# Kernel tuning notes

Measured on AMD Instinct MI355X. Metric: run time of the kernel, lower is better.

Reference implementation:

```python
import jax, jax.numpy as jnp
import numpy as np

B, H, S, D = 2, 16, 2048, 64
DILATION_RATE = 2

def dilated_global_mask(seq_len: int, dilation_rate: int) -> jnp.ndarray:
    # mask[i, j] = 1 if |i - j| % dilation_rate == 0 else 0  -> [S, S] float32
    i = jnp.arange(seq_len)[:, None]
    j = jnp.arange(seq_len)[None, :]
    return ((jnp.abs(i - j) % dilation_rate) == 0).astype(jnp.float32)

def setup_inputs() -> dict:
    key = jax.random.key(0)
    kq, kk, kv = jax.random.split(key, 3)
    queries = jax.random.normal(kq, (B, H, S, D), dtype=jnp.float32)
    keys = jax.random.normal(kk, (B, H, S, D), dtype=jnp.float32)
    values = jax.random.normal(kv, (B, H, S, D), dtype=jnp.float32)
    return {"queries": queries, "keys": keys, "values": values}

def reference(queries, keys, values):
    depth = queries.shape[-1]
    # scores: [B, H, S, S]
    scores = jnp.einsum("bhqd,bhkd->bhqk", queries, keys)
    scores = scores / jnp.sqrt(jnp.asarray(depth, dtype=jnp.float32))
    gmask = dilated_global_mask(keys.shape[-2], DILATION_RATE)  # [S, S]
    # NOTE: multiplicative masking (masked scores become 0, not -inf), as in source
    masked_scores = scores * gmask
    attention_probs = jax.nn.softmax(masked_scores, axis=-1)
    # dropout is identity at inference (training=None)
    out = jnp.einsum("bhqk,bhkd->bhqd", attention_probs, values)
    return out
```

## Files before the change

### kernel.cpp

```cpp
#include <hip/hip_runtime.h>
#include <hip/hip_bf16.h>


#define B_   2
#define H_   16
#define S_   2048
#define D_   64
#define SP_  1024
#define BQ   64
#define BK   64
#define NKT  (SP_ / BK)

#define QSCALE 0.180336884f

#if __has_builtin(__builtin_amdgcn_exp2f)
#define EXP2(x) __builtin_amdgcn_exp2f(x)
#else
#define EXP2(x) exp2f(x)
#endif

typedef __bf16 bf16x8 __attribute__((ext_vector_type(8)));
typedef __bf16 bf16x4 __attribute__((ext_vector_type(4)));
typedef float  f32x4  __attribute__((ext_vector_type(4)));
typedef short  s16x4  __attribute__((ext_vector_type(4)));

static __device__ __forceinline__ f32x4 mfma16(bf16x4 a, bf16x4 b, f32x4 c) {
    return __builtin_amdgcn_mfma_f32_16x16x16bf16_1k(
        __builtin_bit_cast(s16x4, a), __builtin_bit_cast(s16x4, b), c, 0, 0, 0);
}

#define KSW(r, c8) ((((c8) ^ ((r) & 7)) << 3))

__global__ __launch_bounds__(256) void conv_kernel(const float* __restrict__ K,
                                                   const float* __restrict__ V,
                                                   __bf16* __restrict__ Kbf,
                                                   __bf16* __restrict__ Vt,
                                                   float* __restrict__ vsp) {
    const int bp  = blockIdx.x;
    const int kc  = blockIdx.y;
    const int bh  = bp >> 1;
    const int par = bp & 1;
    const int tid = threadIdx.x;
    const float* Kb = K + (size_t)bh * S_ * D_;
    const float* Vb = V + (size_t)bh * S_ * D_;

    __shared__ __align__(16) __bf16 vt[64][80];
    const int row = tid >> 2;
    const int c0  = (tid & 3) * 16;
    const int c8  = (tid & 3) * 2;

    float vsum = 0.f;
    #pragma unroll
    for (int st2 = 0; st2 < 2; ++st2) {
        const int ktile = kc * 2 + st2;
        const int k0 = ktile * 64;
        {
            const float* ks = Kb + (size_t)(par + 2 * (k0 + row)) * D_ + c0;
            const float4 a0 = *(const float4*)(ks);
            const float4 a1 = *(const float4*)(ks + 4);
            const float4 a2 = *(const float4*)(ks + 8);
            const float4 a3 = *(const float4*)(ks + 12);
            bf16x8 w0, w1;
            w0[0] = (__bf16)a0.x; w0[1] = (__bf16)a0.y;
            w0[2] = (__bf16)a0.z; w0[3] = (__bf16)a0.w;
            w0[4] = (__bf16)a1.x; w0[5] = (__bf16)a1.y;
            w0[6] = (__bf16)a1.z; w0[7] = (__bf16)a1.w;
            w1[0] = (__bf16)a2.x; w1[1] = (__bf16)a2.y;
            w1[2] = (__bf16)a2.z; w1[3] = (__bf16)a2.w;
            w1[4] = (__bf16)a3.x; w1[5] = (__bf16)a3.y;
            w1[6] = (__bf16)a3.z; w1[7] = (__bf16)a3.w;
            __bf16* kdst = Kbf + ((size_t)bp * SP_ + k0 + row) * D_;
            *(bf16x8*)&kdst[KSW(row, c8)]     = w0;
            *(bf16x8*)&kdst[KSW(row, c8 + 1)] = w1;
        }
        {
            const float* vsrc = Vb + (size_t)(par + 2 * (k0 + row)) * D_ + c0;
            const float4 a0 = *(const float4*)(vsrc);
            const float4 a1 = *(const float4*)(vsrc + 4);
            const float4 a2 = *(const float4*)(vsrc + 8);
            const float4 a3 = *(const float4*)(vsrc + 12);
            bf16x8 w0, w1;
            w0[0] = (__bf16)a0.x; w0[1] = (__bf16)a0.y;
            w0[2] = (__bf16)a0.z; w0[3] = (__bf16)a0.w;
            w0[4] = (__bf16)a1.x; w0[5] = (__bf16)a1.y;
            w0[6] = (__bf16)a1.z; w0[7] = (__bf16)a1.w;
            w1[0] = (__bf16)a2.x; w1[1] = (__bf16)a2.y;
            w1[2] = (__bf16)a2.z; w1[3] = (__bf16)a2.w;
            w1[4] = (__bf16)a3.x; w1[5] = (__bf16)a3.y;
            w1[6] = (__bf16)a3.z; w1[7] = (__bf16)a3.w;
            *(bf16x8*)&vt[row][c0]     = w0;
            *(bf16x8*)&vt[row][c0 + 8] = w1;
        }
        __syncthreads();
        {
            const int d = row;
            #pragma unroll
            for (int cc2 = 0; cc2 < 2; ++cc2) {
                const int cc = c8 + cc2;
                bf16x8 w;
                float s = 0.f;
                #pragma unroll
                for (int j = 0; j < 8; ++j) {
                    w[j] = vt[cc * 8 + j][d];
                    s += (float)w[j];
                }
                vsum += s;
                __bf16* vdst = Vt + (((size_t)bp * 16 + ktile) * D_ + d) * 64;
                *(bf16x8*)&vdst[KSW(d, cc)] = w;
            }
        }
        __syncthreads();
    }
    vsum += __shfl_down(vsum, 1);
    vsum += __shfl_down(vsum, 2);
    if ((tid & 3) == 0) vsp[((size_t)bp * 8 + blockIdx.y) * 64 + row] = vsum;
}

__global__ __launch_bounds__(256, 4) void attn3_kernel(const float* __restrict__ Q,
                                                       const __bf16* __restrict__ Kbf,
                                                       const __bf16* __restrict__ Vt,
                                                       const float* __restrict__ vsp,
                                                       float* __restrict__ out) {
    const int bh  = blockIdx.x;
    const int par = blockIdx.y;
    const int qt  = blockIdx.z;
    const int bp  = bh * 2 + par;
    const int tid  = threadIdx.x;
    const int lane = tid & 63;
    const int wave = tid >> 6;
    const int l15  = lane & 15;
    const int quad = lane >> 4;

    __shared__ __align__(16) char arena[32768];
    __bf16 (*kbuf)[BK][64] = (__bf16 (*)[BK][64])arena;
    __bf16 (*vbuf)[D_][64] = (__bf16 (*)[D_][64])(arena + 16384);

    const size_t base = (size_t)bh * S_ * D_;

    bf16x8 qf[2];
    {
        const int qrow = qt * BQ + wave * 16 + l15;
        const float* qsrc = Q + base + (size_t)(par + 2 * qrow) * D_ + quad * 8;
        #pragma unroll
        for (int ks = 0; ks < 2; ++ks) {
            const float4 a = *(const float4*)(qsrc + ks * 32);
            const float4 b = *(const float4*)(qsrc + ks * 32 + 4);
            bf16x8 w;
            w[0] = (__bf16)(a.x * QSCALE); w[1] = (__bf16)(a.y * QSCALE);
            w[2] = (__bf16)(a.z * QSCALE); w[3] = (__bf16)(a.w * QSCALE);
            w[4] = (__bf16)(b.x * QSCALE); w[5] = (__bf16)(b.y * QSCALE);
            w[6] = (__bf16)(b.z * QSCALE); w[7] = (__bf16)(b.w * QSCALE);
            qf[ks] = w;
        }
    }

    const uint4* Kt4 = (const uint4*)(Kbf + (size_t)bp * SP_ * D_);
    const uint4* Vt4 = (const uint4*)(Vt  + (size_t)bp * SP_ * D_);
    uint4 sk0, sk1, sv0, sv1;

    auto issue_loads = [&](int kt) {
        const int o = kt * 512 + tid;
        sk0 = Kt4[o]; sk1 = Kt4[o + 256];
        sv0 = Vt4[o]; sv1 = Vt4[o + 256];
    };
    auto stage = [&](int buf) {
        uint4* kd = (uint4*)kbuf[buf];
        uint4* vd = (uint4*)vbuf[buf];
        kd[tid] = sk0; kd[tid + 256] = sk1;
        vd[tid] = sv0; vd[tid + 256] = sv1;
    };

    issue_loads(0);
    stage(0);
    __syncthreads();

    f32x4 acc[4];
    #pragma unroll
    for (int dt = 0; dt < 4; ++dt) acc[dt] = (f32x4){0.f, 0.f, 0.f, 0.f};
    float l_acc = 0.f;

    for (int kt = 0; kt < NKT; ++kt) {
        const int cur = kt & 1;
        const bool pf = (kt + 1 < NKT);

        if (pf) issue_loads(kt + 1);

        const __bf16 (*kb)[64] = kbuf[cur];
        const __bf16 (*vb)[64] = vbuf[cur];

        bf16x8 ka[2][4];
        #pragma unroll
        for (int ks = 0; ks < 2; ++ks)
            #pragma unroll
            for (int kt4 = 0; kt4 < 4; ++kt4) {
                const int R = kt4 * 16 + l15;
                ka[ks][kt4] = *(const bf16x8*)&kb[R][KSW(R, ks * 4 + quad)];
            }
        bf16x4 va[4][4];
        #pragma unroll
        for (int dt = 0; dt < 4; ++dt) {
            const int R = dt * 16 + l15;
            const int ro = R & 7;
            #pragma unroll
            for (int kt4 = 0; kt4 < 4; ++kt4) {
                const int ch = (kt4 * 2 + (quad >> 1)) ^ ro;
                va[kt4][dt] = *(const bf16x4*)&vb[R][ch * 8 + (quad & 1) * 4];
            }
        }

        f32x4 st[4];
        #pragma unroll
        for (int kt4 = 0; kt4 < 4; ++kt4) st[kt4] = (f32x4){0.f, 0.f, 0.f, 0.f};
        #pragma unroll
        for (int ks = 0; ks < 2; ++ks)
            #pragma unroll
            for (int kt4 = 0; kt4 < 4; ++kt4)
                st[kt4] = __builtin_amdgcn_mfma_f32_16x16x32_bf16(
                    ka[ks][kt4], qf[ks], st[kt4], 0, 0, 0);
        #pragma unroll
        for (int kt4 = 0; kt4 < 4; ++kt4) {
            const float p0 = EXP2(st[kt4][0]);
            const float p1 = EXP2(st[kt4][1]);
            const float p2 = EXP2(st[kt4][2]);
            const float p3 = EXP2(st[kt4][3]);
            l_acc += (p0 + p1) + (p2 + p3);
            bf16x4 pb;
            pb[0] = (__bf16)p0; pb[1] = (__bf16)p1;
            pb[2] = (__bf16)p2; pb[3] = (__bf16)p3;
            #pragma unroll
            for (int dt = 0; dt < 4; ++dt)
                acc[dt] = mfma16(va[kt4][dt], pb, acc[dt]);
        }

        if (pf) stage(1 - cur);
        __syncthreads();
    }

    float Z = l_acc;
    Z += __shfl_xor(Z, 16);
    Z += __shfl_xor(Z, 32);
    const float rz = 1.0f / (Z + 1024.0f);

    const float* vsb = vsp + (size_t)(bh * 2 + (1 - par)) * 8 * 64;
    f32x4 vs4[4];
    #pragma unroll
    for (int dt = 0; dt < 4; ++dt) {
        f32x4 s = (f32x4){0.f, 0.f, 0.f, 0.f};
        #pragma unroll
        for (int kc = 0; kc < 8; ++kc)
            s += *(const f32x4*)&vsb[kc * 64 + dt * 16 + quad * 4];
        vs4[dt] = s;
    }

    float* tw = (float*)arena + wave * (16 * 68);
    #pragma unroll
    for (int dt = 0; dt < 4; ++dt) {
        const f32x4 o = (acc[dt] + vs4[dt]) * rz;
        *(f32x4*)&tw[l15 * 68 + dt * 16 + quad * 4] = o;
    }
    #pragma unroll
    for (int i = 0; i < 4; ++i) {
        const int q = i * 4 + quad;
        const f32x4 ov = *(const f32x4*)&tw[q * 68 + l15 * 4];
        const int qg = par + 2 * (qt * BQ + wave * 16 + q);
        *(f32x4*)&out[base + (size_t)qg * D_ + l15 * 4] = ov;
    }
}

__global__ __launch_bounds__(1024) void vsum_kernel(const float* __restrict__ V,
                                                    float* __restrict__ vs) {
    const int bp  = blockIdx.x;
    const int bh  = bp >> 1;
    const int par = bp & 1;
    const int d   = threadIdx.x & 63;
    const int rg  = threadIdx.x >> 6;
    const float* Vb = V + (size_t)bh * S_ * D_;
    float s = 0.f;
    for (int r = rg; r < SP_; r += 16)
        s += Vb[(size_t)(par + 2 * r) * D_ + d];
    __shared__ float red[16][64];
    red[rg][d] = s;
    __syncthreads();
    if (rg == 0) {
        float t = 0.f;
        #pragma unroll
        for (int i = 0; i < 16; ++i) t += red[i][d];
        vs[(size_t)bp * 64 + d] = t;
    }
}

__global__ __launch_bounds__(256, 4) void attn_fb_kernel(const float* __restrict__ Q,
                                                         const float* __restrict__ K,
                                                         const float* __restrict__ V,
                                                         const float* __restrict__ vs,
                                                         float* __restrict__ out) {
    const int bh  = blockIdx.x;
    const int par = blockIdx.y;
    const int qt  = blockIdx.z;
    const int tid  = threadIdx.x;
    const int lane = tid & 63;
    const int wave = tid >> 6;
    const int l15  = lane & 15;
    const int quad = lane >> 4;

    __shared__ __align__(16) char arena[32768];
    __bf16 (*kbuf)[BK][64] = (__bf16 (*)[BK][64])arena;
    __bf16 (*vbuf)[D_][64] = (__bf16 (*)[D_][64])(arena + 16384);

    const size_t base = (size_t)bh * S_ * D_;
    const float* Qb = Q + base;
    const float* Kb = K + base;
    const float* Vb = V + base;

    bf16x8 qf[2];
    {
        const int qrow = qt * BQ + wave * 16 + l15;
        const float* qsrc = Qb + (size_t)(par + 2 * qrow) * D_ + quad * 8;
        #pragma unroll
        for (int ks = 0; ks < 2; ++ks) {
            const float4 a = *(const float4*)(qsrc + ks * 32);
            const float4 b = *(const float4*)(qsrc + ks * 32 + 4);
            bf16x8 w;
            w[0] = (__bf16)(a.x * QSCALE); w[1] = (__bf16)(a.y * QSCALE);
            w[2] = (__bf16)(a.z * QSCALE); w[3] = (__bf16)(a.w * QSCALE);
            w[4] = (__bf16)(b.x * QSCALE); w[5] = (__bf16)(b.y * QSCALE);
            w[6] = (__bf16)(b.z * QSCALE); w[7] = (__bf16)(b.w * QSCALE);
            qf[ks] = w;
        }
    }

    const int kr0 = tid >> 3;
    const int kc8 = tid & 7;
    float4 pka[2], pkb[2];
    float  pv[16];

    auto issue_loads = [&](int kt) {
        #pragma unroll
        for (int i = 0; i < 2; ++i) {
            const int r = i * 32 + kr0;
            const float* ksrc = Kb + (size_t)(par + 2 * (kt * BK + r)) * D_ + kc8 * 8;
            pka[i] = *(const float4*)ksrc;
            pkb[i] = *(const float4*)(ksrc + 4);
        }
        #pragma unroll
        for (int i = 0; i < 2; ++i) {
            const int c = wave + 4 * i;
            const float* vsrc = Vb + (size_t)(par + 2 * (kt * BK + c * 8)) * D_ + lane;
            #pragma unroll
            for (int j = 0; j < 8; ++j)
                pv[i * 8 + j] = vsrc[(size_t)(2 * j) * D_];
        }
    };
    auto stage = [&](int buf) {
        #pragma unroll
        for (int i = 0; i < 2; ++i) {
            const int r = i * 32 + kr0;
            bf16x8 w;
            w[0] = (__bf16)pka[i].x; w[1] = (__bf16)pka[i].y;
            w[2] = (__bf16)pka[i].z; w[3] = (__bf16)pka[i].w;
            w[4] = (__bf16)pkb[i].x; w[5] = (__bf16)pkb[i].y;
            w[6] = (__bf16)pkb[i].z; w[7] = (__bf16)pkb[i].w;
            *(bf16x8*)&kbuf[buf][r][KSW(r, kc8)] = w;
        }
        #pragma unroll
        for (int i = 0; i < 2; ++i) {
            const int c = wave + 4 * i;
            bf16x8 w;
            #pragma unroll
            for (int j = 0; j < 8; ++j) w[j] = (__bf16)pv[i * 8 + j];
            *(bf16x8*)&vbuf[buf][lane][KSW(lane, c)] = w;
        }
    };

    issue_loads(0);
    stage(0);
    __syncthreads();

    f32x4 acc[4];
    #pragma unroll
    for (int dt = 0; dt < 4; ++dt) acc[dt] = (f32x4){0.f, 0.f, 0.f, 0.f};
    float l_acc = 0.f;

    for (int kt = 0; kt < NKT; ++kt) {
        const int cur = kt & 1;
        const bool pf = (kt + 1 < NKT);
        if (pf) issue_loads(kt + 1);

        const __bf16 (*kb)[64] = kbuf[cur];
        const __bf16 (*vb)[64] = vbuf[cur];

        bf16x8 ka[2][4];
        #pragma unroll
        for (int ks = 0; ks < 2; ++ks)
            #pragma unroll
            for (int kt4 = 0; kt4 < 4; ++kt4) {
                const int R = kt4 * 16 + l15;
                ka[ks][kt4] = *(const bf16x8*)&kb[R][KSW(R, ks * 4 + quad)];
            }
        bf16x4 va[4][4];
        #pragma unroll
        for (int dt = 0; dt < 4; ++dt) {
            const int R = dt * 16 + l15;
            const int ro = R & 7;
            #pragma unroll
            for (int kt4 = 0; kt4 < 4; ++kt4) {
                const int ch = (kt4 * 2 + (quad >> 1)) ^ ro;
                va[kt4][dt] = *(const bf16x4*)&vb[R][ch * 8 + (quad & 1) * 4];
            }
        }

        f32x4 st[4];
        #pragma unroll
        for (int kt4 = 0; kt4 < 4; ++kt4) st[kt4] = (f32x4){0.f, 0.f, 0.f, 0.f};
        #pragma unroll
        for (int ks = 0; ks < 2; ++ks)
            #pragma unroll
            for (int kt4 = 0; kt4 < 4; ++kt4)
                st[kt4] = __builtin_amdgcn_mfma_f32_16x16x32_bf16(
                    ka[ks][kt4], qf[ks], st[kt4], 0, 0, 0);
        #pragma unroll
        for (int kt4 = 0; kt4 < 4; ++kt4) {
            const float p0 = EXP2(st[kt4][0]);
            const float p1 = EXP2(st[kt4][1]);
            const float p2 = EXP2(st[kt4][2]);
            const float p3 = EXP2(st[kt4][3]);
            l_acc += (p0 + p1) + (p2 + p3);
            bf16x4 pb;
            pb[0] = (__bf16)p0; pb[1] = (__bf16)p1;
            pb[2] = (__bf16)p2; pb[3] = (__bf16)p3;
            #pragma unroll
            for (int dt = 0; dt < 4; ++dt)
                acc[dt] = mfma16(va[kt4][dt], pb, acc[dt]);
        }

        if (pf) stage(1 - cur);
        __syncthreads();
    }

    float Z = l_acc;
    Z += __shfl_xor(Z, 16);
    Z += __shfl_xor(Z, 32);
    const float rz = 1.0f / (Z + 1024.0f);
    const float* vso = vs + ((size_t)(bh * 2 + (1 - par))) * 64;

    float* tw = (float*)arena + wave * (16 * 68);
    #pragma unroll
    for (int dt = 0; dt < 4; ++dt) {
        const f32x4 vs4 = *(const f32x4*)&vso[dt * 16 + quad * 4];
        const f32x4 o = (acc[dt] + vs4) * rz;
        *(f32x4*)&tw[l15 * 68 + dt * 16 + quad * 4] = o;
    }
    #pragma unroll
    for (int i = 0; i < 4; ++i) {
        const int q = i * 4 + quad;
        const f32x4 ov = *(const f32x4*)&tw[q * 68 + l15 * 4];
        const int qg = par + 2 * (qt * BQ + wave * 16 + q);
        *(f32x4*)&out[base + (size_t)qg * D_ + l15 * 4] = ov;
    }
}

extern "C" void kernel_launch(void* const* d_in, const int* in_sizes, int n_in,
                              void* d_out, int out_size, void* d_ws, size_t ws_size,
                              hipStream_t stream) {
    const float* Q = (const float*)d_in[0];
    const float* K = (const float*)d_in[1];
    const float* V = (const float*)d_in[2];
    float* out = (float*)d_out;

    const size_t KBF_BYTES = (size_t)64 * SP_ * D_ * sizeof(__bf16);
    const size_t VSP_BYTES = (size_t)64 * 8 * 64 * sizeof(float);
    const size_t need = 2 * KBF_BYTES + VSP_BYTES;

    if (ws_size >= need) {
        __bf16* Kbf = (__bf16*)d_ws;
        __bf16* Vt  = (__bf16*)((char*)d_ws + KBF_BYTES);
        float*  vsp = (float*)((char*)d_ws + 2 * KBF_BYTES);
        conv_kernel<<<dim3(64, 8), dim3(256), 0, stream>>>(K, V, Kbf, Vt, vsp);
        attn3_kernel<<<dim3(B_ * H_, 2, SP_ / BQ), dim3(256), 0, stream>>>(
            Q, Kbf, Vt, vsp, out);
    } else {
        float* vsn = (float*)d_ws;
        vsum_kernel<<<dim3(B_ * H_ * 2), dim3(1024), 0, stream>>>(V, vsn);
        attn_fb_kernel<<<dim3(B_ * H_, 2, SP_ / BQ), dim3(256), 0, stream>>>(
            Q, K, V, vsn, out);
    }
}
```

Measured before the change: 125.1 us.

## Use 2-wave blocks with two query sub-tiles per wave and remap grid

The attention kernel now runs 128-thread blocks in which each wave handles 32 query rows as two 16-row sub-tiles. This reuses each K/V fragment read from LDS for twice as many MFMAs, and the staging loop is reorganised so the smaller block still loads the full K/V tile. A 1D grid with a swizzled block-to-(bh,par,qt) mapping spreads neighbouring blocks across head-pairs, and s_setprio raises wave priority around the MFMA section. The cost is higher register pressure from doubled accumulators and fewer waves per block to hide latency.

```diff
diff --git a/kernel.cpp b/kernel.cpp
--- a/kernel.cpp
+++ b/kernel.cpp
@@ -8,6 +8,7 @@
 #define D_   64
 #define SP_  1024
 #define BQ   64
+#define FBQ  64
 #define BK   64
 #define NKT  (SP_ / BK)
 
@@ -116,14 +117,16 @@
     if ((tid & 3) == 0) vsp[((size_t)bp * 8 + blockIdx.y) * 64 + row] = vsum;
 }
 
-__global__ __launch_bounds__(256, 4) void attn3_kernel(const float* __restrict__ Q,
+__global__ __launch_bounds__(128, 2) void attn5_kernel(const float* __restrict__ Q,
                                                        const __bf16* __restrict__ Kbf,
                                                        const __bf16* __restrict__ Vt,
                                                        const float* __restrict__ vsp,
                                                        float* __restrict__ out) {
-    const int bh  = blockIdx.x;
-    const int par = blockIdx.y;
-    const int qt  = blockIdx.z;
+    const int h  = blockIdx.x;
+    const int L  = (h & 7) * 128 + (h >> 3);
+    const int qt  = L & 15;
+    const int par = (L >> 4) & 1;
+    const int bh  = L >> 5;
     const int bp  = bh * 2 + par;
     const int tid  = threadIdx.x;
     const int lane = tid & 63;
@@ -137,9 +140,10 @@
 
     const size_t base = (size_t)bh * S_ * D_;
 
-    bf16x8 qf[2];
-    {
-        const int qrow = qt * BQ + wave * 16 + l15;
+    bf16x8 qf[2][2];
+    #pragma unroll
+    for (int qt2 = 0; qt2 < 2; ++qt2) {
+        const int qrow = qt * BQ + wave * 32 + qt2 * 16 + l15;
         const float* qsrc = Q + base + (size_t)(par + 2 * qrow) * D_ + quad * 8;
         #pragma unroll
         for (int ks = 0; ks < 2; ++ks) {
@@ -150,34 +154,42 @@
             w[2] = (__bf16)(a.z * QSCALE); w[3] = (__bf16)(a.w * QSCALE);
             w[4] = (__bf16)(b.x * QSCALE); w[5] = (__bf16)(b.y * QSCALE);
             w[6] = (__bf16)(b.z * QSCALE); w[7] = (__bf16)(b.w * QSCALE);
-            qf[ks] = w;
+            qf[qt2][ks] = w;
         }
     }
 
     const uint4* Kt4 = (const uint4*)(Kbf + (size_t)bp * SP_ * D_);
     const uint4* Vt4 = (const uint4*)(Vt  + (size_t)bp * SP_ * D_);
-    uint4 sk0, sk1, sv0, sv1;
+    uint4 sk[4], sv[4];
 
     auto issue_loads = [&](int kt) {
-        const int o = kt * 512 + tid;
-        sk0 = Kt4[o]; sk1 = Kt4[o + 256];
-        sv0 = Vt4[o]; sv1 = Vt4[o + 256];
+        #pragma unroll
+        for (int i = 0; i < 4; ++i) {
+            const int o = kt * 512 + tid + i * 128;
+            sk[i] = Kt4[o];
+            sv[i] = Vt4[o];
+        }
     };
     auto stage = [&](int buf) {
         uint4* kd = (uint4*)kbuf[buf];
         uint4* vd = (uint4*)vbuf[buf];
-        kd[tid] = sk0; kd[tid + 256] = sk1;
-        vd[tid] = sv0; vd[tid + 256] = sv1;
+        #pragma unroll
+        for (int i = 0; i < 4; ++i) {
+            kd[tid + i * 128] = sk[i];
+            vd[tid + i * 128] = sv[i];
+        }
     };
 
     issue_loads(0);
     stage(0);
     __syncthreads();
 
-    f32x4 acc[4];
-    #pragma unroll
-    for (int dt = 0; dt < 4; ++dt) acc[dt] = (f32x4){0.f, 0.f, 0.f, 0.f};
-    float l_acc = 0.f;
+    f32x4 acc[2][4];
+    #pragma unroll
+    for (int q2 = 0; q2 < 2; ++q2)
+        #pragma unroll
+        for (int dt = 0; dt < 4; ++dt) acc[q2][dt] = (f32x4){0.f, 0.f, 0.f, 0.f};
+    float l_acc[2] = {0.f, 0.f};
 
     for (int kt = 0; kt < NKT; ++kt) {
         const int cur = kt & 1;
@@ -208,39 +220,47 @@
             }
         }
 
-        f32x4 st[4];
-        #pragma unroll
-        for (int kt4 = 0; kt4 < 4; ++kt4) st[kt4] = (f32x4){0.f, 0.f, 0.f, 0.f};
-        #pragma unroll
-        for (int ks = 0; ks < 2; ++ks)
-            #pragma unroll
-            for (int kt4 = 0; kt4 < 4; ++kt4)
-                st[kt4] = __builtin_amdgcn_mfma_f32_16x16x32_bf16(
-                    ka[ks][kt4], qf[ks], st[kt4], 0, 0, 0);
-        #pragma unroll
-        for (int kt4 = 0; kt4 < 4; ++kt4) {
-            const float p0 = EXP2(st[kt4][0]);
-            const float p1 = EXP2(st[kt4][1]);
-            const float p2 = EXP2(st[kt4][2]);
-            const float p3 = EXP2(st[kt4][3]);
-            l_acc += (p0 + p1) + (p2 + p3);
-            bf16x4 pb;
-            pb[0] = (__bf16)p0; pb[1] = (__bf16)p1;
-            pb[2] = (__bf16)p2; pb[3] = (__bf16)p3;
-            #pragma unroll
-            for (int dt = 0; dt < 4; ++dt)
-                acc[dt] = mfma16(va[kt4][dt], pb, acc[dt]);
-        }
+        __builtin_amdgcn_s_setprio(1);
+        #pragma unroll
+        for (int qt2 = 0; qt2 < 2; ++qt2) {
+            f32x4 st[4];
+            #pragma unroll
+            for (int kt4 = 0; kt4 < 4; ++kt4) st[kt4] = (f32x4){0.f, 0.f, 0.f, 0.f};
+            #pragma unroll
+            for (int ks = 0; ks < 2; ++ks)
+                #pragma unroll
+                for (int kt4 = 0; kt4 < 4; ++kt4)
+                    st[kt4] = __builtin_amdgcn_mfma_f32_16x16x32_bf16(
+                        ka[ks][kt4], qf[qt2][ks], st[kt4], 0, 0, 0);
+            #pragma unroll
+            for (int kt4 = 0; kt4 < 4; ++kt4) {
+                const float p0 = EXP2(st[kt4][0]);
+                const float p1 = EXP2(st[kt4][1]);
+                const float p2 = EXP2(st[kt4][2]);
+                const float p3 = EXP2(st[kt4][3]);
+                l_acc[qt2] += (p0 + p1) + (p2 + p3);
+                bf16x4 pb;
+                pb[0] = (__bf16)p0; pb[1] = (__bf16)p1;
+                pb[2] = (__bf16)p2; pb[3] = (__bf16)p3;
+                #pragma unroll
+                for (int dt = 0; dt < 4; ++dt)
+                    acc[qt2][dt] = mfma16(va[kt4][dt], pb, acc[qt2][dt]);
+            }
+        }
+        __builtin_amdgcn_s_setprio(0);
 
         if (pf) stage(1 - cur);
         __syncthreads();
     }
 
-    float Z = l_acc;
-    Z += __shfl_xor(Z, 16);
-    Z += __shfl_xor(Z, 32);
-    const float rz = 1.0f / (Z + 1024.0f);
-
+    float rz[2];
+    #pragma unroll
+    for (int qt2 = 0; qt2 < 2; ++qt2) {
+        float Z = l_acc[qt2];
+        Z += __shfl_xor(Z, 16);
+        Z += __shfl_xor(Z, 32);
+        rz[qt2] = 1.0f / (Z + 1024.0f);
+    }
     const float* vsb = vsp + (size_t)(bh * 2 + (1 - par)) * 8 * 64;
     f32x4 vs4[4];
     #pragma unroll
@@ -254,16 +274,19 @@
 
     float* tw = (float*)arena + wave * (16 * 68);
     #pragma unroll
-    for (int dt = 0; dt < 4; ++dt) {
-        const f32x4 o = (acc[dt] + vs4[dt]) * rz;
-        *(f32x4*)&tw[l15 * 68 + dt * 16 + quad * 4] = o;
-    }
-    #pragma unroll
-    for (int i = 0; i < 4; ++i) {
-        const int q = i * 4 + quad;
-        const f32x4 ov = *(const f32x4*)&tw[q * 68 + l15 * 4];
-        const int qg = par + 2 * (qt * BQ + wave * 16 + q);
-        *(f32x4*)&out[base + (size_t)qg * D_ + l15 * 4] = ov;
+    for (int qt2 = 0; qt2 < 2; ++qt2) {
+        #pragma unroll
+        for (int dt = 0; dt < 4; ++dt) {
+            const f32x4 o = (acc[qt2][dt] + vs4[dt]) * rz[qt2];
+            *(f32x4*)&tw[l15 * 68 + dt * 16 + quad * 4] = o;
+        }
+        #pragma unroll
+        for (int i = 0; i < 4; ++i) {
+            const int q = i * 4 + quad;
+            const f32x4 ov = *(const f32x4*)&tw[q * 68 + l15 * 4];
+            const int qg = par + 2 * (qt * BQ + wave * 32 + qt2 * 16 + q);
+            *(f32x4*)&out[base + (size_t)qg * D_ + l15 * 4] = ov;
+        }
     }
 }
 
@@ -314,7 +337,7 @@
 
     bf16x8 qf[2];
     {
-        const int qrow = qt * BQ + wave * 16 + l15;
+        const int qrow = qt * FBQ + wave * 16 + l15;
         const float* qsrc = Qb + (size_t)(par + 2 * qrow) * D_ + quad * 8;
         #pragma unroll
         for (int ks = 0; ks < 2; ++ks) {
@@ -454,7 +477,7 @@
     for (int i = 0; i < 4; ++i) {
         const int q = i * 4 + quad;
         const f32x4 ov = *(const f32x4*)&tw[q * 68 + l15 * 4];
-        const int qg = par + 2 * (qt * BQ + wave * 16 + q);
+        const int qg = par + 2 * (qt * FBQ + wave * 16 + q);
         *(f32x4*)&out[base + (size_t)qg * D_ + l15 * 4] = ov;
     }
 }
@@ -476,12 +499,12 @@
         __bf16* Vt  = (__bf16*)((char*)d_ws + KBF_BYTES);
         float*  vsp = (float*)((char*)d_ws + 2 * KBF_BYTES);
         conv_kernel<<<dim3(64, 8), dim3(256), 0, stream>>>(K, V, Kbf, Vt, vsp);
-        attn3_kernel<<<dim3(B_ * H_, 2, SP_ / BQ), dim3(256), 0, stream>>>(
+        attn5_kernel<<<dim3(64 * 16), dim3(128), 0, stream>>>(
             Q, Kbf, Vt, vsp, out);
     } else {
         float* vsn = (float*)d_ws;
         vsum_kernel<<<dim3(B_ * H_ * 2), dim3(1024), 0, stream>>>(V, vsn);
-        attn_fb_kernel<<<dim3(B_ * H_, 2, SP_ / BQ), dim3(256), 0, stream>>>(
+        attn_fb_kernel<<<dim3(B_ * H_, 2, SP_ / FBQ), dim3(256), 0, stream>>>(
             Q, K, V, vsn, out);
     }
 }
```

After: 158.6 us. 26.7% more time.
